# Optimization experiments

Measured on AMD Instinct MI355X. Metric: run time of the kernel, lower is better.

## Reference

```python
import jax, jax.numpy as jnp
import numpy as np

DIM = 1280
HEADS = 16
HEAD_DIM = DIM // HEADS  # 80
N_CHUNKS = 8
CHUNK = 1024
TOTAL = N_CHUNKS * CHUNK  # 8192 packed tokens


def rotate_half(x):
    x1, x2 = jnp.split(x, 2, axis=-1)
    return jnp.concatenate([-x2, x1], axis=-1)


def setup_inputs() -> dict:
    key = jax.random.key(0)
    k0, k1, k2 = jax.random.split(key, 3)
    hidden_states = jax.random.normal(k0, (TOTAL, DIM), dtype=jnp.float32)
    # 2D-rope style per-token angles, duplicated halves (standard vision RoPE layout)
    inv_freq = 1.0 / (10000.0 ** (jnp.arange(0, HEAD_DIM, 2, dtype=jnp.float32) / HEAD_DIM))
    pos = jnp.arange(TOTAL, dtype=jnp.float32)
    freqs = pos[:, None] * inv_freq[None, :]            # [T, HEAD_DIM//2]
    emb = jnp.concatenate([freqs, freqs], axis=-1)      # [T, HEAD_DIM]
    cos = jnp.cos(emb)
    sin = jnp.sin(emb)
    qkv_w = jax.random.normal(k1, (3 * DIM, DIM), dtype=jnp.float32) * 0.02
    qkv_b = jnp.zeros((3 * DIM,), dtype=jnp.float32)
    proj_w = jax.random.normal(k2, (DIM, DIM), dtype=jnp.float32) * 0.02
    proj_b = jnp.zeros((DIM,), dtype=jnp.float32)
    cu_seqlens = (jnp.arange(N_CHUNKS + 1, dtype=jnp.int32) * CHUNK)
    return {"hidden_states": hidden_states, "cos": cos, "sin": sin,
            "qkv_w": qkv_w, "qkv_b": qkv_b, "proj_w": proj_w, "proj_b": proj_b,
            "cu_seqlens": cu_seqlens}


def reference(hidden_states, cos, sin, qkv_w, qkv_b, proj_w, proj_b, cu_seqlens):
    # Equal-length chunks (cu_seqlens uniform): vectorize the Python chunk loop
    # as a leading batch axis n over chunks of length L.
    n = cu_seqlens.shape[0] - 1
    total, dim = hidden_states.shape
    L = total // n
    scaling = HEAD_DIM ** -0.5

    x = hidden_states.reshape(n, L, dim)
    qkv = x @ qkv_w.T + qkv_b                              # [n, L, 3*dim]
    qkv = qkv.reshape(n, L, 3, HEADS, HEAD_DIM)
    q, k, v = qkv[:, :, 0], qkv[:, :, 1], qkv[:, :, 2]     # [n, L, H, hd]

    # inline RoPE in fp32 (matches apply_rotary_pos_emb_vision)
    c = cos.reshape(n, L, 1, HEAD_DIM).astype(jnp.float32)
    s = sin.reshape(n, L, 1, HEAD_DIM).astype(jnp.float32)
    qf = q.astype(jnp.float32)
    kf = k.astype(jnp.float32)
    q = (qf * c + rotate_half(qf) * s).astype(q.dtype)
    k = (kf * c + rotate_half(kf) * s).astype(k.dtype)

    # naive per-chunk full attention: QK^T, fp32 softmax, PV
    scores = jnp.einsum('nlhd,nmhd->nhlm', q, k) * scaling  # [n, H, L, L]
    probs = jax.nn.softmax(scores.astype(jnp.float32), axis=-1).astype(q.dtype)
    out = jnp.einsum('nhlm,nmhd->nlhd', probs, v)           # [n, L, H, hd]
    out = out.reshape(n, L, dim)
    out = out @ proj_w.T + proj_b                           # [n, L, dim]
    return out.reshape(total, dim)
```

## Files before the change

kernel.cpp:

```cpp
#include <hip/hip_runtime.h>
#include <stdint.h>

#define DIM 1280
#define HEADS 16
#define HD 80
#define TOTAL 8192
#define CHUNK 1024
#define QKVN 3840

typedef __attribute__((ext_vector_type(8))) __bf16 bf16x8;
typedef __attribute__((ext_vector_type(4))) float floatx4;

typedef __attribute__((address_space(1))) const uint32_t gu32;
typedef __attribute__((address_space(3))) uint32_t lu32;

__device__ __forceinline__ void llds16(const void* g, void* l) {
  __builtin_amdgcn_global_load_lds((gu32*)g, (lu32*)l, 16, 0, 0);
}

__device__ __forceinline__ unsigned short f2b(float f) {
  union { __bf16 b; unsigned short u; } x; x.b = (__bf16)f; return x.u;
}
__device__ __forceinline__ float b2f(unsigned short u) {
  union { __bf16 b; unsigned short u; } x; x.u = u; return (float)x.b;
}
__device__ __forceinline__ float fexp2(float x) {
#if __has_builtin(__builtin_amdgcn_exp2f)
  return __builtin_amdgcn_exp2f(x);
#else
  return __expf(x * 0.6931471805599453f);
#endif
}

#define QSCALE (0.11180339887498949f * 1.44269504088896340f)

#define QROW 96
#define KT_SH (64 * 104)
#define VT_SH (80 * 72)

__global__ void cvt_bf16(const float* __restrict__ src, unsigned short* __restrict__ dst, int n4) {
  int i = blockIdx.x * 256 + threadIdx.x;
  if (i >= n4) return;
  float4 v = reinterpret_cast<const float4*>(src)[i];
  ushort4 o;
  o.x = f2b(v.x); o.y = f2b(v.y); o.z = f2b(v.z); o.w = f2b(v.w);
  reinterpret_cast<ushort4*>(dst)[i] = o;
}


__device__ __forceinline__ void stage_a64(const unsigned short* __restrict__ G,
                                          unsigned short* ls, int wv, int lane,
                                          int row0, int kk, int hi) {
#pragma unroll
  for (int t = 0; t < 2; ++t) {
    const int stripe = t * 8 + wv;
    const int rb = ((stripe >> 3) << 7) + ((stripe & 7) << 3) + hi;
    const int r = rb + (lane >> 3);
    const int ch = (lane & 7) ^ (r & 7);
    llds16(G + (size_t)(row0 + r) * DIM + kk + (ch << 3), ls + rb * 64);
  }
}

__device__ __forceinline__ void stage_b64(const unsigned short* __restrict__ G,
                                          unsigned short* ls, int wv, int lane,
                                          int row0, int kk, int hi) {
#pragma unroll
  for (int t = 0; t < 2; ++t) {
    const int stripe = t * 8 + wv;
    const int rb = ((stripe >> 2) << 6) + ((stripe & 3) << 3) + hi;
    const int r = rb + (lane >> 3);
    const int ch = (lane & 7) ^ (r & 7);
    llds16(G + (size_t)(row0 + r) * DIM + kk + (ch << 3), ls + rb * 64);
  }
}

__device__ __forceinline__ bf16x8 frg(const unsigned short* ls, int r, int cx) {
  return *reinterpret_cast<const bf16x8*>(ls + r * 64 + (cx << 3));
}

#define PH_PRE()                                          \
  __builtin_amdgcn_s_barrier();                           \
  asm volatile("s_waitcnt lgkmcnt(0)" ::: "memory");      \
  __builtin_amdgcn_sched_barrier(0);                      \
  __builtin_amdgcn_s_setprio(1)

#define PH_POST() __builtin_amdgcn_s_setprio(0)

template<int MODE>
__launch_bounds__(512, 2)
__global__ void gemm8(const unsigned short* __restrict__ A,
                      const unsigned short* __restrict__ B,
                      const float* __restrict__ bias,
                      unsigned short* __restrict__ qo,
                      unsigned short* __restrict__ ko,
                      unsigned short* __restrict__ vo,
                      float* __restrict__ fo) {
  __shared__ __attribute__((aligned(16))) unsigned short lsA[2][256 * 64];
  __shared__ __attribute__((aligned(16))) unsigned short lsB[2][256 * 64];
  const int m0 = blockIdx.x * 256;
  const int n0 = blockIdx.y * 256;
  const int tid = threadIdx.x;
  const int wv = tid >> 6, lane = tid & 63;
  const int wr = wv >> 2, wc = wv & 3;
  const int q4 = lane >> 4, l15 = lane & 15;
  const int sx = l15 & 7;
  const int cx0 = q4 ^ sx;
  const int cx1 = (4 + q4) ^ sx;

  stage_a64(A, &lsA[0][0], wv, lane, m0, 0, 0);
  stage_b64(B, &lsB[0][0], wv, lane, n0, 0, 0);
  stage_b64(B, &lsB[0][0], wv, lane, n0, 0, 32);
  stage_a64(A, &lsA[0][0], wv, lane, m0, 0, 64);

  floatx4 acc[8][4];
#pragma unroll
  for (int i = 0; i < 8; ++i)
#pragma unroll
    for (int j = 0; j < 4; ++j)
      acc[i][j] = (floatx4){0.f, 0.f, 0.f, 0.f};

  asm volatile("s_waitcnt vmcnt(4)" ::: "memory");
  __builtin_amdgcn_s_barrier();

  const int rA = wr * 128 + l15;
  const int rB = wc * 64 + l15;

#pragma unroll 2
  for (int kt = 0; kt < 20; ++kt) {
    const unsigned short* la = &lsA[kt & 1][0];
    const unsigned short* lb = &lsB[kt & 1][0];
    unsigned short* sa = &lsA[(kt & 1) ^ 1][0];
    unsigned short* sb = &lsB[(kt & 1) ^ 1][0];
    const int kn = (kt + 1) * 64;
    const bool st = (kt < 19);

    bf16x8 Ar[4][2], Br[2][2];

#pragma unroll
    for (int m = 0; m < 4; ++m) {
      Ar[m][0] = frg(la, rA + m * 16, cx0);
      Ar[m][1] = frg(la, rA + m * 16, cx1);
    }
#pragma unroll
    for (int n = 0; n < 2; ++n) {
      Br[n][0] = frg(lb, rB + n * 16, cx0);
      Br[n][1] = frg(lb, rB + n * 16, cx1);
    }
    if (st) stage_a64(A, sa, wv, lane, m0, kn, 0);
    PH_PRE();
#pragma unroll
    for (int m = 0; m < 4; ++m)
#pragma unroll
      for (int n = 0; n < 2; ++n) {
        acc[m][n] = __builtin_amdgcn_mfma_f32_16x16x32_bf16(Ar[m][0], Br[n][0], acc[m][n], 0, 0, 0);
        acc[m][n] = __builtin_amdgcn_mfma_f32_16x16x32_bf16(Ar[m][1], Br[n][1], acc[m][n], 0, 0, 0);
      }
    PH_POST();
    if (st) asm volatile("s_waitcnt vmcnt(4)" ::: "memory");
    else    asm volatile("s_waitcnt vmcnt(2)" ::: "memory");
    __builtin_amdgcn_s_barrier();

#pragma unroll
    for (int n = 0; n < 2; ++n) {
      Br[n][0] = frg(lb, rB + (n + 2) * 16, cx0);
      Br[n][1] = frg(lb, rB + (n + 2) * 16, cx1);
    }
    if (st) stage_b64(B, sb, wv, lane, n0, kn, 0);
    PH_PRE();
#pragma unroll
    for (int m = 0; m < 4; ++m)
#pragma unroll
      for (int n = 0; n < 2; ++n) {
        acc[m][n + 2] = __builtin_amdgcn_mfma_f32_16x16x32_bf16(Ar[m][0], Br[n][0], acc[m][n + 2], 0, 0, 0);
        acc[m][n + 2] = __builtin_amdgcn_mfma_f32_16x16x32_bf16(Ar[m][1], Br[n][1], acc[m][n + 2], 0, 0, 0);
      }
    PH_POST();
    if (st) asm volatile("s_waitcnt vmcnt(4)" ::: "memory");
    else    asm volatile("s_waitcnt vmcnt(0)" ::: "memory");
    __builtin_amdgcn_s_barrier();

#pragma unroll
    for (int m = 0; m < 4; ++m) {
      Ar[m][0] = frg(la, rA + (m + 4) * 16, cx0);
      Ar[m][1] = frg(la, rA + (m + 4) * 16, cx1);
    }
    if (st) stage_b64(B, sb, wv, lane, n0, kn, 32);
    PH_PRE();
#pragma unroll
    for (int m = 0; m < 4; ++m)
#pragma unroll
      for (int n = 0; n < 2; ++n) {
        acc[m + 4][n + 2] = __builtin_amdgcn_mfma_f32_16x16x32_bf16(Ar[m][0], Br[n][0], acc[m + 4][n + 2], 0, 0, 0);
        acc[m + 4][n + 2] = __builtin_amdgcn_mfma_f32_16x16x32_bf16(Ar[m][1], Br[n][1], acc[m + 4][n + 2], 0, 0, 0);
      }
    PH_POST();
    __builtin_amdgcn_s_barrier();

#pragma unroll
    for (int n = 0; n < 2; ++n) {
      Br[n][0] = frg(lb, rB + n * 16, cx0);
      Br[n][1] = frg(lb, rB + n * 16, cx1);
    }
    if (st) stage_a64(A, sa, wv, lane, m0, kn, 64);
    PH_PRE();
#pragma unroll
    for (int m = 0; m < 4; ++m)
#pragma unroll
      for (int n = 0; n < 2; ++n) {
        acc[m + 4][n] = __builtin_amdgcn_mfma_f32_16x16x32_bf16(Ar[m][0], Br[n][0], acc[m + 4][n], 0, 0, 0);
        acc[m + 4][n] = __builtin_amdgcn_mfma_f32_16x16x32_bf16(Ar[m][1], Br[n][1], acc[m + 4][n], 0, 0, 0);
      }
    PH_POST();
    if (st) asm volatile("s_waitcnt vmcnt(4)" ::: "memory");
    __builtin_amdgcn_s_barrier();
  }

  unsigned short* os = nullptr;
  int nloc = n0;
  if (MODE == 0) {
    if (blockIdx.y < 5)       { os = qo; }
    else if (blockIdx.y < 10) { os = ko; nloc = n0 - DIM; }
    else                      { os = vo; nloc = n0 - 2 * DIM; }
  }
#pragma unroll
  for (int n = 0; n < 4; ++n) {
    const int cg = wc * 64 + n * 16 + l15;
    const float bn = bias[n0 + cg];
#pragma unroll
    for (int m = 0; m < 8; ++m) {
#pragma unroll
      for (int r = 0; r < 4; ++r) {
        const int row = m0 + wr * 128 + m * 16 + q4 * 4 + r;
        const float val = acc[m][n][r] + bn;
        if (MODE == 0) os[(size_t)row * DIM + nloc + cg] = f2b(val);
        else           fo[(size_t)row * DIM + n0 + cg] = val;
      }
    }
  }
}

__global__ void prep_q(const unsigned short* __restrict__ qbuf,
                       const float* __restrict__ cp, const float* __restrict__ sp,
                       unsigned short* __restrict__ qimg) {
  const int m = blockIdx.x, tid = threadIdx.x;
  const int ch = m >> 10, rl = m & 1023;
#pragma unroll
  for (int i = 0; i < 3; ++i) {
    const int it = i * 256 + tid;
    if (it < 640) {
      const int h = it / 40, d = it - h * 40;
      const float c = cp[m * HD + d], s = sp[m * HD + d];
      const float x1 = b2f(qbuf[(size_t)m * DIM + h * HD + d]);
      const float x2 = b2f(qbuf[(size_t)m * DIM + h * HD + d + 40]);
      const size_t ob = ((size_t)(ch * 16 + h) * 1024 + rl) * QROW;
      qimg[ob + d]      = f2b((x1 * c - x2 * s) * QSCALE);
      qimg[ob + d + 40] = f2b((x2 * c + x1 * s) * QSCALE);
    }
  }
  { const int h = tid >> 4, c = tid & 15;
    qimg[((size_t)(ch * 16 + h) * 1024 + rl) * QROW + 80 + c] = 0; }
}

__global__ void prep_k(const unsigned short* __restrict__ kbuf,
                       const float* __restrict__ cp, const float* __restrict__ sp,
                       unsigned short* __restrict__ kimg) {
  const int m = blockIdx.x, tid = threadIdx.x;
  const int ch = m >> 10, rl = m & 1023;
  const int jt = rl >> 6, rr = rl & 63;
#pragma unroll
  for (int i = 0; i < 3; ++i) {
    const int it = i * 256 + tid;
    if (it < 640) {
      const int h = it / 40, d = it - h * 40;
      const float c = cp[m * HD + d], s = sp[m * HD + d];
      const float x1 = b2f(kbuf[(size_t)m * DIM + h * HD + d]);
      const float x2 = b2f(kbuf[(size_t)m * DIM + h * HD + d + 40]);
      const size_t ob = ((size_t)((ch * 16 + h) * 16 + jt) * KT_SH) + rr * 104;
      kimg[ob + d]      = f2b(x1 * c - x2 * s);
      kimg[ob + d + 40] = f2b(x2 * c + x1 * s);
    }
  }
#pragma unroll
  for (int i = 0; i < 2; ++i) {
    const int it = i * 256 + tid;
    if (it < 384) {
      const int h = it / 24, c = it - h * 24;
      kimg[((size_t)((ch * 16 + h) * 16 + jt) * KT_SH) + rr * 104 + 80 + c] = 0;
    }
  }
}

__global__ void prep_v(const unsigned short* __restrict__ vbuf,
                       unsigned short* __restrict__ vimg) {
  __shared__ __attribute__((aligned(16))) unsigned short lsT[64 * 88];
  const int bx = blockIdx.x;
  const int jt = bx & 15, h = (bx >> 4) & 15, ch = bx >> 8;
  const int tid = threadIdx.x;
  const int row0 = ch * CHUNK + jt * 64;
#pragma unroll
  for (int i = 0; i < 3; ++i) {
    const int it = i * 256 + tid;
    if (it < 640) {
      const int r = it / 10, c = it - r * 10;
      const uint4 v = *reinterpret_cast<const uint4*>(vbuf + (size_t)(row0 + r) * DIM + h * HD + c * 8);
      *reinterpret_cast<uint4*>(&lsT[r * 88 + c * 8]) = v;
    }
  }
  __syncthreads();
  unsigned short* ot = vimg + (size_t)((ch * 16 + h) * 16 + jt) * VT_SH;
#pragma unroll
  for (int i = 0; i < 12; ++i) {
    const int it = i * 256 + tid;
    if (it < 2880) {
      const int d = it / 36, kk = it - d * 36;
      uint32_t w = 0;
      if (kk < 32) {
        const uint32_t lo = lsT[(2 * kk) * 88 + d];
        const uint32_t hi = lsT[(2 * kk + 1) * 88 + d];
        w = lo | (hi << 16);
      }
      *reinterpret_cast<uint32_t*>(ot + d * 72 + kk * 2) = w;
    }
  }
}

__launch_bounds__(256, 3)
__global__ void attn_k(const unsigned short* __restrict__ qimg,
                       const unsigned short* __restrict__ kimg,
                       const unsigned short* __restrict__ vimg,
                       unsigned short* __restrict__ ob) {
  __shared__ __attribute__((aligned(16))) unsigned short lsK[KT_SH];
  __shared__ __attribute__((aligned(16))) unsigned short lsV[VT_SH];
  __shared__ __attribute__((aligned(16))) unsigned short lsP[128 * 72];

  const int bx = blockIdx.x;
  const int qt = bx & 7, h = (bx >> 3) & 15, ch = bx >> 7;
  const int tid = threadIdx.x, wv = tid >> 6, lane = tid & 63;
  const int q4 = lane >> 4, l15 = lane & 15;
  const int qrow_loc = qt * 128 + wv * 32;

  bf16x8 aq[2][3];
  {
    const unsigned short* qb = qimg + ((size_t)(ch * 16 + h) * 1024 + qrow_loc) * QROW;
#pragma unroll
    for (int mt = 0; mt < 2; ++mt)
#pragma unroll
      for (int ks = 0; ks < 3; ++ks)
        aq[mt][ks] = *reinterpret_cast<const bf16x8*>(qb + (size_t)(mt * 16 + l15) * QROW + ks * 32 + q4 * 8);
  }

  floatx4 oacc[2][5];
  float lpart[2] = {0.f, 0.f};
#pragma unroll
  for (int mt = 0; mt < 2; ++mt)
#pragma unroll
    for (int t = 0; t < 5; ++t) oacc[mt][t] = (floatx4){0.f, 0.f, 0.f, 0.f};

  const char* kbase = (const char*)(kimg + (size_t)(ch * 16 + h) * 16 * KT_SH);
  const char* vbase = (const char*)(vimg + (size_t)(ch * 16 + h) * 16 * VT_SH);

  for (int jt = 0; jt < 16; ++jt) {
    __syncthreads();
    {
      const char* kg = kbase + (size_t)jt * (KT_SH * 2);
#pragma unroll
      for (int r = 0; r < 4; ++r) {
        const int off = (r * 4 + wv) * 1024;
        if (off < KT_SH * 2)
          llds16(kg + off + lane * 16, (char*)lsK + off);
      }
      const char* vg = vbase + (size_t)jt * (VT_SH * 2);
#pragma unroll
      for (int r = 0; r < 3; ++r) {
        const int off = (r * 4 + wv) * 1024;
        if (off < VT_SH * 2) {
          if (off + 1024 <= VT_SH * 2) llds16(vg + off + lane * 16, (char*)lsV + off);
          else if (lane < 16)          llds16(vg + off + lane * 16, (char*)lsV + off);
        }
      }
    }
    __syncthreads();

    floatx4 sfr[2][4];
#pragma unroll
    for (int c = 0; c < 4; ++c) {
      const bf16x8 ak0 = *reinterpret_cast<const bf16x8*>(&lsK[(c * 16 + l15) * 104 + 0  + q4 * 8]);
      const bf16x8 ak1 = *reinterpret_cast<const bf16x8*>(&lsK[(c * 16 + l15) * 104 + 32 + q4 * 8]);
      const bf16x8 ak2 = *reinterpret_cast<const bf16x8*>(&lsK[(c * 16 + l15) * 104 + 64 + q4 * 8]);
#pragma unroll
      for (int mt = 0; mt < 2; ++mt) {
        floatx4 s = (floatx4){0.f, 0.f, 0.f, 0.f};
        s = __builtin_amdgcn_mfma_f32_16x16x32_bf16(ak0, aq[mt][0], s, 0, 0, 0);
        s = __builtin_amdgcn_mfma_f32_16x16x32_bf16(ak1, aq[mt][1], s, 0, 0, 0);
        s = __builtin_amdgcn_mfma_f32_16x16x32_bf16(ak2, aq[mt][2], s, 0, 0, 0);
        sfr[mt][c] = s;
      }
    }

#pragma unroll
    for (int mt = 0; mt < 2; ++mt)
#pragma unroll
      for (int c = 0; c < 4; ++c) {
        const float p0 = fexp2(sfr[mt][c][0]);
        const float p1 = fexp2(sfr[mt][c][1]);
        const float p2 = fexp2(sfr[mt][c][2]);
        const float p3 = fexp2(sfr[mt][c][3]);
        lpart[mt] += (p0 + p1) + (p2 + p3);
        ushort4 w;
        w.x = f2b(p0); w.y = f2b(p1); w.z = f2b(p2); w.w = f2b(p3);
        *reinterpret_cast<ushort4*>(&lsP[(wv * 32 + mt * 16 + l15) * 72 + c * 16 + q4 * 4]) = w;
      }

#pragma unroll
    for (int ks = 0; ks < 2; ++ks) {
      const bf16x8 ap0 = *reinterpret_cast<const bf16x8*>(&lsP[(wv * 32 + 0  + l15) * 72 + ks * 32 + q4 * 8]);
      const bf16x8 ap1 = *reinterpret_cast<const bf16x8*>(&lsP[(wv * 32 + 16 + l15) * 72 + ks * 32 + q4 * 8]);
#pragma unroll
      for (int t = 0; t < 5; ++t) {
        const bf16x8 bv = *reinterpret_cast<const bf16x8*>(&lsV[(t * 16 + l15) * 72 + ks * 32 + q4 * 8]);
        oacc[0][t] = __builtin_amdgcn_mfma_f32_16x16x32_bf16(ap0, bv, oacc[0][t], 0, 0, 0);
        oacc[1][t] = __builtin_amdgcn_mfma_f32_16x16x32_bf16(ap1, bv, oacc[1][t], 0, 0, 0);
      }
    }
  }

#pragma unroll
  for (int mt = 0; mt < 2; ++mt) {
    lpart[mt] += __shfl_xor(lpart[mt], 16, 64);
    lpart[mt] += __shfl_xor(lpart[mt], 32, 64);
  }
  float inv[2];
  inv[0] = 1.0f / lpart[0];
  inv[1] = 1.0f / lpart[1];

  float invr[2][4];
#pragma unroll
  for (int mt = 0; mt < 2; ++mt)
#pragma unroll
    for (int r = 0; r < 4; ++r)
      invr[mt][r] = __shfl(inv[mt], q4 * 4 + r, 64);

#pragma unroll
  for (int mt = 0; mt < 2; ++mt)
#pragma unroll
    for (int t = 0; t < 5; ++t)
#pragma unroll
      for (int r = 0; r < 4; ++r) {
        const int gr = ch * CHUNK + qrow_loc + mt * 16 + q4 * 4 + r;
        const int gc = h * HD + t * 16 + l15;
        ob[(size_t)gr * DIM + gc] = f2b(oacc[mt][t][r] * invr[mt][r]);
      }
}

extern "C" void kernel_launch(void* const* d_in, const int* in_sizes, int n_in,
                              void* d_out, int out_size, void* d_ws, size_t ws_size,
                              hipStream_t stream) {
  (void)in_sizes; (void)n_in; (void)out_size; (void)ws_size;
  const float* hs    = (const float*)d_in[0];
  const float* cosp  = (const float*)d_in[1];
  const float* sinp  = (const float*)d_in[2];
  const float* qkvw  = (const float*)d_in[3];
  const float* qkvb  = (const float*)d_in[4];
  const float* projw = (const float*)d_in[5];
  const float* projb = (const float*)d_in[6];

  char* ws = (char*)d_ws;
  unsigned short* xb   = (unsigned short*)(ws + 0);
  unsigned short* wq   = (unsigned short*)(ws + 20971520);
  unsigned short* qbuf = (unsigned short*)(ws + 30801920);
  unsigned short* kbuf = (unsigned short*)(ws + 51773440);
  unsigned short* vbuf = (unsigned short*)(ws + 72744960);
  unsigned short* wp   = (unsigned short*)(ws + 93716480);
  unsigned short* obuf = (unsigned short*)(ws + 96993280);
  unsigned short* kimg = (unsigned short*)(ws + 117964800);
  unsigned short* qimg = (unsigned short*)(ws + 0);
  unsigned short* vimg = (unsigned short*)(ws + 30801920);

  cvt_bf16<<<TOTAL * DIM / 4 / 256, 256, 0, stream>>>(hs, xb, TOTAL * DIM / 4);
  cvt_bf16<<<QKVN * DIM / 4 / 256, 256, 0, stream>>>(qkvw, wq, QKVN * DIM / 4);
  cvt_bf16<<<DIM * DIM / 4 / 256, 256, 0, stream>>>(projw, wp, DIM * DIM / 4);

  gemm8<0><<<dim3(TOTAL / 256, QKVN / 256), 512, 0, stream>>>(
      xb, wq, qkvb, qbuf, kbuf, vbuf, nullptr);

  prep_q<<<TOTAL, 256, 0, stream>>>(qbuf, cosp, sinp, qimg);
  prep_k<<<TOTAL, 256, 0, stream>>>(kbuf, cosp, sinp, kimg);
  prep_v<<<2048, 256, 0, stream>>>(vbuf, vimg);

  attn_k<<<1024, 256, 0, stream>>>(qimg, kimg, vimg, obuf);

  gemm8<1><<<dim3(TOTAL / 256, DIM / 256), 512, 0, stream>>>(
      obuf, wp, projb, nullptr, nullptr, nullptr, (float*)d_out);
}
```

Measured before the change: 380.3 us.

## Deepen GEMM prefetch to two k-tiles ahead and keep B fragments in registers

Restructures the 8-wave GEMM main loop so global-to-LDS loads are issued two k-steps ahead, writing into the current buffer once its fragments are consumed, instead of one step ahead. B fragments are kept in separate low and high register sets, which removes one LDS reload per iteration and one barrier phase. The goal is to hide global memory latency behind more MFMA work and cut LDS traffic. In exchange it needs more VGPRs and relies on subtle vmcnt and barrier ordering, which risks races or register spills.

```diff
diff --git a/kernel.cpp b/kernel.cpp
--- a/kernel.cpp
+++ b/kernel.cpp
@@ -78,13 +78,7 @@
   return *reinterpret_cast<const bf16x8*>(ls + r * 64 + (cx << 3));
 }
 
-#define PH_PRE()                                          \
-  __builtin_amdgcn_s_barrier();                           \
-  asm volatile("s_waitcnt lgkmcnt(0)" ::: "memory");      \
-  __builtin_amdgcn_sched_barrier(0);                      \
-  __builtin_amdgcn_s_setprio(1)
-
-#define PH_POST() __builtin_amdgcn_s_setprio(0)
+#define MFMA_BF16 __builtin_amdgcn_mfma_f32_16x16x32_bf16
 
 template<int MODE>
 __launch_bounds__(512, 2)
@@ -111,6 +105,9 @@
   stage_b64(B, &lsB[0][0], wv, lane, n0, 0, 0);
   stage_b64(B, &lsB[0][0], wv, lane, n0, 0, 32);
   stage_a64(A, &lsA[0][0], wv, lane, m0, 0, 64);
+  stage_b64(B, &lsB[1][0], wv, lane, n0, 64, 0);
+  stage_a64(A, &lsA[1][0], wv, lane, m0, 64, 0);
+  stage_b64(B, &lsB[1][0], wv, lane, n0, 64, 32);
 
   floatx4 acc[8][4];
 #pragma unroll
@@ -119,7 +116,7 @@
     for (int j = 0; j < 4; ++j)
       acc[i][j] = (floatx4){0.f, 0.f, 0.f, 0.f};
 
-  asm volatile("s_waitcnt vmcnt(4)" ::: "memory");
+  asm volatile("s_waitcnt vmcnt(6)" ::: "memory");
   __builtin_amdgcn_s_barrier();
 
   const int rA = wr * 128 + l15;
@@ -129,12 +126,13 @@
   for (int kt = 0; kt < 20; ++kt) {
     const unsigned short* la = &lsA[kt & 1][0];
     const unsigned short* lb = &lsB[kt & 1][0];
-    unsigned short* sa = &lsA[(kt & 1) ^ 1][0];
-    unsigned short* sb = &lsB[(kt & 1) ^ 1][0];
-    const int kn = (kt + 1) * 64;
-    const bool st = (kt < 19);
-
-    bf16x8 Ar[4][2], Br[2][2];
+    unsigned short* aN = &lsA[(kt & 1) ^ 1][0];
+    unsigned short* aC = &lsA[kt & 1][0];
+    unsigned short* bC = &lsB[kt & 1][0];
+    const bool st1 = (kt + 1 < 20);
+    const bool st2 = (kt + 2 < 20);
+
+    bf16x8 Ar[4][2], Blo[2][2], Bhi[2][2];
 
 #pragma unroll
     for (int m = 0; m < 4; ++m) {
@@ -143,40 +141,43 @@
     }
 #pragma unroll
     for (int n = 0; n < 2; ++n) {
-      Br[n][0] = frg(lb, rB + n * 16, cx0);
-      Br[n][1] = frg(lb, rB + n * 16, cx1);
-    }
-    if (st) stage_a64(A, sa, wv, lane, m0, kn, 0);
-    PH_PRE();
+      Blo[n][0] = frg(lb, rB + n * 16, cx0);
+      Blo[n][1] = frg(lb, rB + n * 16, cx1);
+    }
+    if (st1) stage_a64(A, aN, wv, lane, m0, (kt + 1) * 64, 64);
+    asm volatile("s_waitcnt lgkmcnt(8)" ::: "memory");
+    __builtin_amdgcn_s_barrier();
+    asm volatile("s_waitcnt lgkmcnt(0)" ::: "memory");
+    __builtin_amdgcn_sched_barrier(0);
+    __builtin_amdgcn_s_setprio(1);
 #pragma unroll
     for (int m = 0; m < 4; ++m)
 #pragma unroll
       for (int n = 0; n < 2; ++n) {
-        acc[m][n] = __builtin_amdgcn_mfma_f32_16x16x32_bf16(Ar[m][0], Br[n][0], acc[m][n], 0, 0, 0);
-        acc[m][n] = __builtin_amdgcn_mfma_f32_16x16x32_bf16(Ar[m][1], Br[n][1], acc[m][n], 0, 0, 0);
-      }
-    PH_POST();
-    if (st) asm volatile("s_waitcnt vmcnt(4)" ::: "memory");
-    else    asm volatile("s_waitcnt vmcnt(2)" ::: "memory");
+        acc[m][n] = MFMA_BF16(Ar[m][0], Blo[n][0], acc[m][n], 0, 0, 0);
+        acc[m][n] = MFMA_BF16(Ar[m][1], Blo[n][1], acc[m][n], 0, 0, 0);
+      }
+    __builtin_amdgcn_s_setprio(0);
     __builtin_amdgcn_s_barrier();
 
 #pragma unroll
     for (int n = 0; n < 2; ++n) {
-      Br[n][0] = frg(lb, rB + (n + 2) * 16, cx0);
-      Br[n][1] = frg(lb, rB + (n + 2) * 16, cx1);
-    }
-    if (st) stage_b64(B, sb, wv, lane, n0, kn, 0);
-    PH_PRE();
+      Bhi[n][0] = frg(lb, rB + (n + 2) * 16, cx0);
+      Bhi[n][1] = frg(lb, rB + (n + 2) * 16, cx1);
+    }
+    if (st2) stage_b64(B, bC, wv, lane, n0, (kt + 2) * 64, 0);
+    __builtin_amdgcn_s_barrier();
+    asm volatile("s_waitcnt lgkmcnt(0)" ::: "memory");
+    __builtin_amdgcn_sched_barrier(0);
+    __builtin_amdgcn_s_setprio(1);
 #pragma unroll
     for (int m = 0; m < 4; ++m)
 #pragma unroll
       for (int n = 0; n < 2; ++n) {
-        acc[m][n + 2] = __builtin_amdgcn_mfma_f32_16x16x32_bf16(Ar[m][0], Br[n][0], acc[m][n + 2], 0, 0, 0);
-        acc[m][n + 2] = __builtin_amdgcn_mfma_f32_16x16x32_bf16(Ar[m][1], Br[n][1], acc[m][n + 2], 0, 0, 0);
-      }
-    PH_POST();
-    if (st) asm volatile("s_waitcnt vmcnt(4)" ::: "memory");
-    else    asm volatile("s_waitcnt vmcnt(0)" ::: "memory");
+        acc[m][n + 2] = MFMA_BF16(Ar[m][0], Bhi[n][0], acc[m][n + 2], 0, 0, 0);
+        acc[m][n + 2] = MFMA_BF16(Ar[m][1], Bhi[n][1], acc[m][n + 2], 0, 0, 0);
+      }
+    __builtin_amdgcn_s_setprio(0);
     __builtin_amdgcn_s_barrier();
 
 #pragma unroll
@@ -184,35 +185,35 @@
       Ar[m][0] = frg(la, rA + (m + 4) * 16, cx0);
       Ar[m][1] = frg(la, rA + (m + 4) * 16, cx1);
     }
-    if (st) stage_b64(B, sb, wv, lane, n0, kn, 32);
-    PH_PRE();
+    if (st2) stage_a64(A, aC, wv, lane, m0, (kt + 2) * 64, 0);
+    __builtin_amdgcn_s_barrier();
+    asm volatile("s_waitcnt lgkmcnt(0)" ::: "memory");
+    __builtin_amdgcn_sched_barrier(0);
+    __builtin_amdgcn_s_setprio(1);
 #pragma unroll
     for (int m = 0; m < 4; ++m)
 #pragma unroll
       for (int n = 0; n < 2; ++n) {
-        acc[m + 4][n + 2] = __builtin_amdgcn_mfma_f32_16x16x32_bf16(Ar[m][0], Br[n][0], acc[m + 4][n + 2], 0, 0, 0);
-        acc[m + 4][n + 2] = __builtin_amdgcn_mfma_f32_16x16x32_bf16(Ar[m][1], Br[n][1], acc[m + 4][n + 2], 0, 0, 0);
-      }
-    PH_POST();
-    __builtin_amdgcn_s_barrier();
-
-#pragma unroll
-    for (int n = 0; n < 2; ++n) {
-      Br[n][0] = frg(lb, rB + n * 16, cx0);
-      Br[n][1] = frg(lb, rB + n * 16, cx1);
-    }
-    if (st) stage_a64(A, sa, wv, lane, m0, kn, 64);
-    PH_PRE();
+        acc[m + 4][n + 2] = MFMA_BF16(Ar[m][0], Bhi[n][0], acc[m + 4][n + 2], 0, 0, 0);
+        acc[m + 4][n + 2] = MFMA_BF16(Ar[m][1], Bhi[n][1], acc[m + 4][n + 2], 0, 0, 0);
+      }
+    __builtin_amdgcn_s_setprio(0);
+    __builtin_amdgcn_s_barrier();
+
+    if (st2) stage_b64(B, bC, wv, lane, n0, (kt + 2) * 64, 32);
+    __builtin_amdgcn_s_setprio(1);
 #pragma unroll
     for (int m = 0; m < 4; ++m)
 #pragma unroll
       for (int n = 0; n < 2; ++n) {
-        acc[m + 4][n] = __builtin_amdgcn_mfma_f32_16x16x32_bf16(Ar[m][0], Br[n][0], acc[m + 4][n], 0, 0, 0);
-        acc[m + 4][n] = __builtin_amdgcn_mfma_f32_16x16x32_bf16(Ar[m][1], Br[n][1], acc[m + 4][n], 0, 0, 0);
-      }
-    PH_POST();
-    if (st) asm volatile("s_waitcnt vmcnt(4)" ::: "memory");
-    __builtin_amdgcn_s_barrier();
+        acc[m + 4][n] = MFMA_BF16(Ar[m][0], Blo[n][0], acc[m + 4][n], 0, 0, 0);
+        acc[m + 4][n] = MFMA_BF16(Ar[m][1], Blo[n][1], acc[m + 4][n], 0, 0, 0);
+      }
+    __builtin_amdgcn_s_setprio(0);
+
+    if (st2)      asm volatile("s_waitcnt vmcnt(6)" ::: "memory");
+    else if (st1) asm volatile("s_waitcnt vmcnt(0)" ::: "memory");
+    if (st1) __builtin_amdgcn_s_barrier();
   }
 
   unsigned short* os = nullptr;
```

Result: faster. 362.0 us (-4.8%).
